# Kernel tuning notes

Hardware: AMD Instinct MI355X
Metric: run time of the kernel (lower is better)

The kernel has to match this reference:

```python
import jax, jax.numpy as jnp
import numpy as np

N_NODES = 50000
N_EDGES = 1600000


def _glorot(key, shape):
    fan_in, fan_out = shape[-1], int(np.prod(shape[:-1]))
    limit = float(np.sqrt(6.0 / (fan_in + fan_out)))
    return jax.random.uniform(key, shape, jnp.float32, -limit, limit)


def setup_inputs() -> dict:
    key = jax.random.key(0)
    ks = jax.random.split(key, 10)
    x = jax.random.normal(ks[0], (N_NODES, 128), jnp.float32)
    edge_index = jax.random.randint(ks[1], (2, N_EDGES), 0, N_NODES, jnp.int64 if jax.config.jax_enable_x64 else jnp.int32)
    # Layer 1: in=128, heads=8, out=8 (concat -> 64)
    W1 = _glorot(ks[2], (8 * 8, 128))          # [H*F, F_in]
    a_src1 = _glorot(ks[3], (1, 8, 8))
    a_trg1 = _glorot(ks[4], (1, 8, 8))
    b1 = jnp.zeros((8 * 8,), jnp.float32)
    # Layer 2: in=64, heads=1, out=7 (mean -> 7)
    W2 = _glorot(ks[5], (1 * 7, 64))
    a_src2 = _glorot(ks[6], (1, 1, 7))
    a_trg2 = _glorot(ks[7], (1, 1, 7))
    b2 = jnp.zeros((7,), jnp.float32)
    return {"x": x, "edge_index": edge_index, "W1": W1, "a_src1": a_src1,
            "a_trg1": a_trg1, "b1": b1, "W2": W2, "a_src2": a_src2,
            "a_trg2": a_trg2, "b2": b2}


def _segment_softmax(scores, seg, num_segments):
    # scores: [E, H], seg: [E] target-node ids. Numerically-stable softmax per segment.
    m = jax.ops.segment_max(scores, seg, num_segments=num_segments)
    e = jnp.exp(scores - m[seg])
    s = jax.ops.segment_sum(e, seg, num_segments=num_segments)
    return e / (s[seg] + 1e-16)


def _gat_layer(x, edge_index, W, a_src, a_trg, bias, concat, activation):
    N = x.shape[0]
    H, F = a_src.shape[1], a_src.shape[2]
    proj = (x @ W.T).reshape(N, H, F)                 # [N, H, F]
    s_src = jnp.sum(proj * a_src, axis=-1)            # [N, H]
    s_trg = jnp.sum(proj * a_trg, axis=-1)            # [N, H]
    src, trg = edge_index[0], edge_index[1]
    scores = jax.nn.leaky_relu(s_src[src] + s_trg[trg], 0.2)   # [E, H]
    att = _segment_softmax(scores, trg, N)            # [E, H]
    msg = proj[src] * att[..., None]                  # [E, H, F]
    out = jax.ops.segment_sum(msg, trg, num_segments=N)  # [N, H, F]
    out = out.reshape(N, H * F) if concat else out.mean(axis=1)
    return activation(out + bias)


def reference(x, edge_index, W1, a_src1, a_trg1, b1, W2, a_src2, a_trg2, b2):
    # Dropout is identity at inference.
    h = _gat_layer(x, edge_index, W1, a_src1, a_trg1, b1, concat=True, activation=jax.nn.elu)
    out = _gat_layer(h, edge_index, W2, a_src2, a_trg2, b2, concat=False,
                     activation=lambda z: jax.nn.softmax(z, axis=-1))
    return out
```

## Files before the change

kernel.cpp:

```cpp
#include <hip/hip_runtime.h>
#include <hip/hip_fp16.h>
#include <math.h>


#define PAD 96
#define NRANGE 4

__device__ __forceinline__ float leaky02(float v){ return v > 0.f ? v : 0.2f*v; }
__device__ __forceinline__ float expc(float v){ return __expf(fminf(v, 60.f)); }

__device__ __forceinline__ int edge_lo(const void* ei, int isI32, long long idx){
  if (isI32) return ((const int*)ei)[idx];
  return ((const int*)ei)[2*idx];
}

__global__ void k_detect(const unsigned int* __restrict__ w, int nwords, int* __restrict__ flag){
  int gid = blockIdx.x*256 + threadIdx.x;
  int stride = gridDim.x*256;
  unsigned int v = 0;
  for (int idx = 2*gid + 1; idx < nwords; idx += 2*stride)
    v |= w[idx];
  unsigned long long b = __ballot(v != 0);
  if ((threadIdx.x & 63) == 0 && b != 0ULL) atomicOr(flag, 1);
}

__global__ void k_scatter_pad(const void* __restrict__ ei, const int* __restrict__ flag,
                              int* __restrict__ cnt, unsigned short* __restrict__ padded,
                              int E, int N, int nch){
  int r  = blockIdx.x & (NRANGE-1);
  int c  = blockIdx.x / NRANGE;
  int lo = (int)((long long)E * c / nch);
  int hi = (int)((long long)E * (c+1) / nch);
  int rngw = (N + NRANGE-1) / NRANGE;
  int tlo = r * rngw, thi = min(tlo + rngw, N);
  int f = *flag;
  for (int e = lo + (int)threadIdx.x; e < hi; e += 256){
    int t = edge_lo(ei, f, (long long)e + E);
    t = min(max(t, 0), N-1);
    if (t < tlo || t >= thi) continue;
    int s = edge_lo(ei, f, (long long)e);
    s = min(max(s, 0), N-1);
    int slot = atomicAdd(&cnt[t], 1);
    if (slot < PAD) padded[(size_t)t*PAD + slot] = (unsigned short)s;
  }
}

__global__ __launch_bounds__(256) void k_gemm1(
    const float* __restrict__ x, const float* __restrict__ W,
    const float* __restrict__ a_src, const float* __restrict__ a_trg,
    __half* __restrict__ proj, float* __restrict__ s_src, float* __restrict__ s_trg, int n){
  const int LP = 68;
  __shared__ float xsT[64*LP];
  __shared__ float wT [64*LP];
  int tid = threadIdx.x;
  int n0  = blockIdx.x*64;
  int tn = tid & 15, tm = tid >> 4;
  const float4* x4 = (const float4*)x;
  float acc[4][4] = {};

  for (int kh = 0; kh < 2; ++kh){
    __syncthreads();
    #pragma unroll
    for (int it=0; it<16; ++it){
      int idx = it*256 + tid;
      int c = idx >> 6, k = idx & 63;
      wT[k*LP + c] = W[c*128 + kh*64 + k];
    }
    #pragma unroll
    for (int it=0; it<4; ++it){
      int idx = it*256 + tid;
      int r = idx >> 4, k4 = idx & 15;
      int row = n0 + r;
      float4 v = (row < n) ? x4[(size_t)row*32 + kh*16 + k4] : make_float4(0.f,0.f,0.f,0.f);
      xsT[(k4*4+0)*LP + r] = v.x;
      xsT[(k4*4+1)*LP + r] = v.y;
      xsT[(k4*4+2)*LP + r] = v.z;
      xsT[(k4*4+3)*LP + r] = v.w;
    }
    __syncthreads();

    #pragma unroll 8
    for (int k=0; k<64; ++k){
      float4 av = *(const float4*)&xsT[k*LP + tm*4];
      float4 bv = *(const float4*)&wT [k*LP + tn*4];
      float a_[4] = {av.x, av.y, av.z, av.w};
      float b_[4] = {bv.x, bv.y, bv.z, bv.w};
      #pragma unroll
      for (int i=0;i<4;++i)
        #pragma unroll
        for (int j=0;j<4;++j)
          acc[i][j] += a_[i]*b_[j];
    }
  }

  float as[4], at[4];
  #pragma unroll
  for (int j=0;j<4;++j){ as[j] = a_src[tn*4+j]; at[j] = a_trg[tn*4+j]; }
  #pragma unroll
  for (int i=0;i<4;++i){
    int row = n0 + tm*4 + i;
    float ps = 0.f, pt = 0.f;
    #pragma unroll
    for (int j=0;j<4;++j){ ps += acc[i][j]*as[j]; pt += acc[i][j]*at[j]; }
    ps += __shfl_xor(ps, 1);
    pt += __shfl_xor(pt, 1);
    if (row < n){
      __half* pr = proj + (size_t)row*64 + tn*4;
      #pragma unroll
      for (int j=0;j<4;++j) pr[j] = __float2half(acc[i][j]);
      if ((tn & 1) == 0){
        s_src[row*8 + (tn>>1)] = ps;
        s_trg[row*8 + (tn>>1)] = pt;
      }
    }
  }
}

__global__ __launch_bounds__(64) void k_agg1f(
    const int* __restrict__ cnt, const unsigned short* __restrict__ padded,
    const float* __restrict__ ss, const float* __restrict__ st,
    const __half* __restrict__ proj, const float* __restrict__ b1,
    const float* __restrict__ W2, const float* __restrict__ as2, const float* __restrict__ at2,
    float* __restrict__ proj2, float* __restrict__ ssrc2, float* __restrict__ strg2, int N){
  int t = blockIdx.x;
  int lane = threadIdx.x;
  const unsigned short* srcs = padded + (size_t)t*PAD;
  int deg = min(cnt[t], PAD);

  int h2 = lane >> 3;
  float st2 = st[t*8 + h2];
  float a0=0.f, a1=0.f, a2=0.f, a3=0.f;
  float d0=0.f, d1=0.f, d2=0.f, d3=0.f;
  int e = 0;
  for (; e + 4 <= deg; e += 4){
    int s0 = min((int)srcs[e+0], N-1);
    int s1 = min((int)srcs[e+1], N-1);
    int s2 = min((int)srcs[e+2], N-1);
    int s3 = min((int)srcs[e+3], N-1);
    float p0 = __half2float(proj[(size_t)s0*64 + lane]);
    float p1 = __half2float(proj[(size_t)s1*64 + lane]);
    float p2 = __half2float(proj[(size_t)s2*64 + lane]);
    float p3 = __half2float(proj[(size_t)s3*64 + lane]);
    float w0 = expc(leaky02(ss[s0*8 + h2] + st2));
    float w1 = expc(leaky02(ss[s1*8 + h2] + st2));
    float w2 = expc(leaky02(ss[s2*8 + h2] + st2));
    float w3 = expc(leaky02(ss[s3*8 + h2] + st2));
    a0 += w0*p0; d0 += w0;
    a1 += w1*p1; d1 += w1;
    a2 += w2*p2; d2 += w2;
    a3 += w3*p3; d3 += w3;
  }
  for (; e < deg; ++e){
    int s0 = min((int)srcs[e], N-1);
    float w0 = expc(leaky02(ss[s0*8 + h2] + st2));
    a0 += w0 * __half2float(proj[(size_t)s0*64 + lane]);
    d0 += w0;
  }
  float den = (d0 + d1) + (d2 + d3);
  float acc = (a0 + a1) + (a2 + a3);
  float z = acc / (den + 1e-16f) + b1[lane];
  z = (z > 0.f) ? z : expm1f(z);

  float pf[7];
  #pragma unroll
  for (int f = 0; f < 7; ++f){
    float v = z * W2[f*64 + lane];
    v += __shfl_xor(v, 1);
    v += __shfl_xor(v, 2);
    v += __shfl_xor(v, 4);
    v += __shfl_xor(v, 8);
    v += __shfl_xor(v, 16);
    v += __shfl_xor(v, 32);
    pf[f] = v;
  }
  if (lane == 0){
    float vs = 0.f, vt = 0.f;
    #pragma unroll
    for (int f = 0; f < 7; ++f){
      proj2[(size_t)t*8 + f] = pf[f];
      vs += pf[f] * as2[f];
      vt += pf[f] * at2[f];
    }
    proj2[(size_t)t*8 + 7] = 0.f;
    ssrc2[t] = vs;
    strg2[t] = vt;
  }
}

__global__ __launch_bounds__(64) void k_agg2(
    const int* __restrict__ cnt, const unsigned short* __restrict__ padded,
    const float* __restrict__ ss, const float* __restrict__ st,
    const float* __restrict__ proj2, const float* __restrict__ b2,
    float* __restrict__ out, int N){
  int t = blockIdx.x;
  int lane = threadIdx.x;
  const unsigned short* srcs = padded + (size_t)t*PAD;
  int deg = min(cnt[t], PAD);
  float stv = st[t];

  int f = lane & 7, g = lane >> 3;
  float a0 = 0.f, a1 = 0.f, d0 = 0.f, d1 = 0.f;
  int e = g;
  for (; e + 8 < deg; e += 16){
    int s0 = min((int)srcs[e], N-1);
    int s1 = min((int)srcs[e+8], N-1);
    float w0 = expc(leaky02(ss[s0] + stv));
    float w1 = expc(leaky02(ss[s1] + stv));
    a0 += w0 * proj2[(size_t)s0*8 + f]; d0 += w0;
    a1 += w1 * proj2[(size_t)s1*8 + f]; d1 += w1;
  }
  if (e < deg){
    int s0 = min((int)srcs[e], N-1);
    float w0 = expc(leaky02(ss[s0] + stv));
    a0 += w0 * proj2[(size_t)s0*8 + f]; d0 += w0;
  }
  float acc = a0 + a1, den = d0 + d1;
  acc += __shfl_xor(acc, 8);  den += __shfl_xor(den, 8);
  acc += __shfl_xor(acc, 16); den += __shfl_xor(den, 16);
  acc += __shfl_xor(acc, 32); den += __shfl_xor(den, 32);

  float z = (f < 7) ? acc / (den + 1e-16f) + b2[f] : -3.0e38f;
  float m = z;
  m = fmaxf(m, __shfl_xor(m, 1));
  m = fmaxf(m, __shfl_xor(m, 2));
  m = fmaxf(m, __shfl_xor(m, 4));
  float ev = (f < 7) ? __expf(z - m) : 0.f;
  float sum = ev;
  sum += __shfl_xor(sum, 1);
  sum += __shfl_xor(sum, 2);
  sum += __shfl_xor(sum, 4);
  if (lane < 7) out[(size_t)t*7 + lane] = ev / sum;
}

extern "C" void kernel_launch(void* const* d_in, const int* in_sizes, int n_in,
                              void* d_out, int out_size, void* d_ws, size_t ws_size,
                              hipStream_t stream){
  int N = in_sizes[0] / 128;
  int E = in_sizes[1] / 2;
  const float* x   = (const float*)d_in[0];
  const void*  ei  = d_in[1];
  const float* W1  = (const float*)d_in[2];
  const float* as1 = (const float*)d_in[3];
  const float* at1 = (const float*)d_in[4];
  const float* b1  = (const float*)d_in[5];
  const float* W2  = (const float*)d_in[6];
  const float* as2 = (const float*)d_in[7];
  const float* at2 = (const float*)d_in[8];
  const float* b2  = (const float*)d_in[9];
  float* out = (float*)d_out;

  auto aln = [](size_t v){ return (v + 255) & ~(size_t)255; };
  char* w = (char*)d_ws;
  int* flag              = (int*)w;            w += aln(4);
  int* cnt               = (int*)w;            w += aln((size_t)N*4);
  unsigned short* padded = (unsigned short*)w; w += aln((size_t)N*PAD*2);
  __half* proj1          = (__half*)w;         w += aln((size_t)N*64*2);
  float* ssrc1           = (float*)w;          w += aln((size_t)N*8*4);
  float* strg1           = (float*)w;          w += aln((size_t)N*8*4);
  float* proj2           = (float*)w;          w += aln((size_t)N*8*4);
  float* ssrc2           = (float*)w;          w += aln((size_t)N*4);
  float* strg2           = (float*)w;          w += aln((size_t)N*4);

  hipMemsetAsync(flag, 0, 4, stream);
  hipMemsetAsync(cnt, 0, (size_t)N*4, stream);

  int nch = 512;

  k_detect     <<<512, 256, 0, stream>>>((const unsigned int*)ei, 2*E, flag);
  k_scatter_pad<<<nch*NRANGE, 256, 0, stream>>>(ei, flag, cnt, padded, E, N, nch);

  k_gemm1<<<(N+63)/64, 256, 0, stream>>>(x, W1, as1, at1, proj1, ssrc1, strg1, N);
  k_agg1f<<<N, 64, 0, stream>>>(cnt, padded, ssrc1, strg1, proj1, b1,
                                W2, as2, at2, proj2, ssrc2, strg2, N);
  k_agg2 <<<N, 64, 0, stream>>>(cnt, padded, ssrc2, strg2, proj2, b2, out, N);
}
```

Measured before the change: 218.3 us.

## Distribute per-edge attention weights across lanes with shuffles and trim detection scan

In layer-1 aggregation, each lane now computes one edge's attention weight per head for a batch of 8 edges, and the weights and source ids are broadcast with shuffles. This replaces computing the same exp in all 8 lanes of a head, and the denominator is reduced across lanes at the end. It also removes the index clamps and the exp clamp, and uses a branchless leaky ReLU. The int64 detection kernel now scans only a prefix of the edge words with fewer blocks. These trade redundant exp and clamp work for shuffle overhead, and they lose robustness against out-of-range indices, large scores, and int64 detection when the high words are zero in the scanned prefix.

Measured after the change: 198.0 us. 1.1x faster.

```diff
diff --git a/kernel.cpp b/kernel.cpp
--- a/kernel.cpp
+++ b/kernel.cpp
@@ -6,8 +6,7 @@
 #define PAD 96
 #define NRANGE 4
 
-__device__ __forceinline__ float leaky02(float v){ return v > 0.f ? v : 0.2f*v; }
-__device__ __forceinline__ float expc(float v){ return __expf(fminf(v, 60.f)); }
+__device__ __forceinline__ float leaky02(float v){ return fmaxf(v, 0.2f*v); }
 
 __device__ __forceinline__ int edge_lo(const void* ei, int isI32, long long idx){
   if (isI32) return ((const int*)ei)[idx];
@@ -127,38 +126,36 @@
   const unsigned short* srcs = padded + (size_t)t*PAD;
   int deg = min(cnt[t], PAD);
 
-  int h2 = lane >> 3;
-  float st2 = st[t*8 + h2];
-  float a0=0.f, a1=0.f, a2=0.f, a3=0.f;
-  float d0=0.f, d1=0.f, d2=0.f, d3=0.f;
+  int j = lane & 7;
+  int h = lane >> 3;
+  float sth = st[t*8 + h];
+
+  float acc = 0.f;
+  float dd  = 0.f;
+
   int e = 0;
-  for (; e + 4 <= deg; e += 4){
-    int s0 = min((int)srcs[e+0], N-1);
-    int s1 = min((int)srcs[e+1], N-1);
-    int s2 = min((int)srcs[e+2], N-1);
-    int s3 = min((int)srcs[e+3], N-1);
-    float p0 = __half2float(proj[(size_t)s0*64 + lane]);
-    float p1 = __half2float(proj[(size_t)s1*64 + lane]);
-    float p2 = __half2float(proj[(size_t)s2*64 + lane]);
-    float p3 = __half2float(proj[(size_t)s3*64 + lane]);
-    float w0 = expc(leaky02(ss[s0*8 + h2] + st2));
-    float w1 = expc(leaky02(ss[s1*8 + h2] + st2));
-    float w2 = expc(leaky02(ss[s2*8 + h2] + st2));
-    float w3 = expc(leaky02(ss[s3*8 + h2] + st2));
-    a0 += w0*p0; d0 += w0;
-    a1 += w1*p1; d1 += w1;
-    a2 += w2*p2; d2 += w2;
-    a3 += w3*p3; d3 += w3;
+  for (; e + 8 <= deg; e += 8){
+    int sj = (int)srcs[e + j];
+    float w = __expf(leaky02(ss[sj*8 + h] + sth));
+    dd += w;
+    #pragma unroll
+    for (int jj = 0; jj < 8; ++jj){
+      int sjj  = __shfl(sj, jj);
+      float ww = __shfl(w, (lane & 56) | jj);
+      acc += ww * __half2float(proj[(size_t)sjj*64 + lane]);
+    }
   }
   for (; e < deg; ++e){
-    int s0 = min((int)srcs[e], N-1);
-    float w0 = expc(leaky02(ss[s0*8 + h2] + st2));
-    a0 += w0 * __half2float(proj[(size_t)s0*64 + lane]);
-    d0 += w0;
-  }
-  float den = (d0 + d1) + (d2 + d3);
-  float acc = (a0 + a1) + (a2 + a3);
-  float z = acc / (den + 1e-16f) + b1[lane];
+    int s0 = (int)srcs[e];
+    float w0 = __expf(leaky02(ss[s0*8 + h] + sth));
+    if (j == 0) dd += w0;
+    acc += w0 * __half2float(proj[(size_t)s0*64 + lane]);
+  }
+  dd += __shfl_xor(dd, 1);
+  dd += __shfl_xor(dd, 2);
+  dd += __shfl_xor(dd, 4);
+
+  float z = acc / (dd + 1e-16f) + b1[lane];
   z = (z > 0.f) ? z : expm1f(z);
 
   float pf[7];
@@ -202,16 +199,16 @@
   float a0 = 0.f, a1 = 0.f, d0 = 0.f, d1 = 0.f;
   int e = g;
   for (; e + 8 < deg; e += 16){
-    int s0 = min((int)srcs[e], N-1);
-    int s1 = min((int)srcs[e+8], N-1);
-    float w0 = expc(leaky02(ss[s0] + stv));
-    float w1 = expc(leaky02(ss[s1] + stv));
+    int s0 = (int)srcs[e];
+    int s1 = (int)srcs[e+8];
+    float w0 = __expf(leaky02(ss[s0] + stv));
+    float w1 = __expf(leaky02(ss[s1] + stv));
     a0 += w0 * proj2[(size_t)s0*8 + f]; d0 += w0;
     a1 += w1 * proj2[(size_t)s1*8 + f]; d1 += w1;
   }
   if (e < deg){
-    int s0 = min((int)srcs[e], N-1);
-    float w0 = expc(leaky02(ss[s0] + stv));
+    int s0 = (int)srcs[e];
+    float w0 = __expf(leaky02(ss[s0] + stv));
     a0 += w0 * proj2[(size_t)s0*8 + f]; d0 += w0;
   }
   float acc = a0 + a1, den = d0 + d1;
@@ -265,8 +262,9 @@
   hipMemsetAsync(cnt, 0, (size_t)N*4, stream);
 
   int nch = 512;
-
-  k_detect     <<<512, 256, 0, stream>>>((const unsigned int*)ei, 2*E, flag);
+  int dwords = min(2*E, 1 << 21);
+
+  k_detect     <<<64, 256, 0, stream>>>((const unsigned int*)ei, dwords, flag);
   k_scatter_pad<<<nch*NRANGE, 256, 0, stream>>>(ei, flag, cnt, padded, E, N, nch);
 
   k_gemm1<<<(N+63)/64, 256, 0, stream>>>(x, W1, as1, at1, proj1, ssrc1, strg1, N);
```
